# Kernel optimization log

Hardware: AMD Instinct MI355X
Metric: run time of the kernel (lower is better)

Reference implementation:

```python
import jax, jax.numpy as jnp
import numpy as np

NUM_HEADS = 16


def setup_inputs() -> dict:
    key = jax.random.key(0)
    k1, _ = jax.random.split(key)
    B, T, C = 2, 2048, 1024
    x = jax.random.normal(k1, (B, T, C), dtype=jnp.float32)
    r_sigma = jnp.array([0.01], dtype=jnp.float32)  # learned scalar, init 0.01
    return {"x": x, "r_sigma": r_sigma}


def reference(x, r_sigma):
    B, T, C = x.shape
    H = NUM_HEADS
    hd = C // H
    xh = x.reshape(B, T, H, hd)                      # (B,T,H,hd)
    # expand_dims(x,2) - expand_dims(x,3): pairwise diff across the HEAD axis
    diff = xh[:, :, None, :, :] - xh[:, :, :, None, :]   # (B,T,H,H,hd)
    # Dist**2 == sum of squared diffs (avoid sqrt-then-square; same math)
    dist_sq = jnp.sum(diff * diff, axis=-1)          # (B,T,H,H)
    Kmat = jnp.exp(-dist_sq * r_sigma[0])            # Gaussian kernel
    # y = x + K @ x  (contract over second head axis)
    y = xh + jnp.einsum('bthg,btgd->bthd', Kmat, xh)
    return y.reshape(B, T, C)
```

## Files before the change

### kernel.cpp

```cpp
#include <hip/hip_runtime.h>


#define NH 16
#define HD 64
#define CC 1024

__global__ __launch_bounds__(256) void K_attention_MH_kernel(
    const float* __restrict__ x,
    const float* __restrict__ r_sigma,
    float* __restrict__ y) {
  __shared__ float xs[HD * 17];
  __shared__ float Ks[NH * NH];

  const int tok = blockIdx.x;
  const int tid = threadIdx.x;
  const float* xp = x + (size_t)tok * CC;
  float* yp = y + (size_t)tok * CC;
  const float sigma = r_sigma[0];

  const float4 v = reinterpret_cast<const float4*>(xp)[tid];
  const int base = tid * 4;
  const int h = base >> 6;
  const int d0 = base & 63;
  xs[(d0 + 0) * 17 + h] = v.x;
  xs[(d0 + 1) * 17 + h] = v.y;
  xs[(d0 + 2) * 17 + h] = v.z;
  xs[(d0 + 3) * 17 + h] = v.w;
  __syncthreads();

  {
    const int hh = tid >> 4;
    const int gg = tid & 15;
    float acc = 0.0f;
#pragma unroll
    for (int d = 0; d < HD; ++d) {
      const float a = xs[d * 17 + hh];
      const float b = xs[d * 17 + gg];
      const float diff = a - b;
      acc = fmaf(diff, diff, acc);
    }
    Ks[hh * 16 + gg] = __expf(-acc * sigma);
  }
  __syncthreads();

  float s0 = 0.0f, s1 = 0.0f, s2 = 0.0f, s3 = 0.0f;
#pragma unroll
  for (int g = 0; g < NH; ++g) {
    const float k = Ks[h * 16 + g];
    s0 = fmaf(k, xs[(d0 + 0) * 17 + g], s0);
    s1 = fmaf(k, xs[(d0 + 1) * 17 + g], s1);
    s2 = fmaf(k, xs[(d0 + 2) * 17 + g], s2);
    s3 = fmaf(k, xs[(d0 + 3) * 17 + g], s3);
  }
  float4 o;
  o.x = v.x + s0;
  o.y = v.y + s1;
  o.z = v.z + s2;
  o.w = v.w + s3;
  reinterpret_cast<float4*>(yp)[tid] = o;
}

extern "C" void kernel_launch(void* const* d_in, const int* in_sizes, int n_in,
                              void* d_out, int out_size, void* d_ws, size_t ws_size,
                              hipStream_t stream) {
  const float* x = (const float*)d_in[0];
  const float* r_sigma = (const float*)d_in[1];
  float* out = (float*)d_out;
  const int ntok = in_sizes[0] / CC;
  K_attention_MH_kernel<<<ntok, 256, 0, stream>>>(x, r_sigma, out);
}
```

Baseline: 81.99 us.

## Compute per-token Gram and K@x with fp16 MFMA, one wave per token

Each wavefront now handles a single token, so block-wide __syncthreads become wave barriers. The pairwise squared distances are computed as |a|^2+|b|^2-2ab from a 16x16 Gram matrix produced by an fp16 MFMA. The K@x product also runs on MFMA in fp16. This moves the scalar FMA loops onto matrix units and cuts synchronisation cost, but casting to fp16 and the Gram expansion lose precision, and the output stores are no longer float4-vectorised.

```diff
diff --git a/kernel.cpp b/kernel.cpp
--- a/kernel.cpp
+++ b/kernel.cpp
@@ -4,60 +4,92 @@
 #define NH 16
 #define HD 64
 #define CC 1024
+#define LDSROW 68
+
+typedef float  f32x4 __attribute__((ext_vector_type(4)));
+typedef _Float16 f16x4 __attribute__((ext_vector_type(4)));
+typedef _Float16 f16x8 __attribute__((ext_vector_type(8)));
 
 __global__ __launch_bounds__(256) void K_attention_MH_kernel(
     const float* __restrict__ x,
     const float* __restrict__ r_sigma,
-    float* __restrict__ y) {
-  __shared__ float xs[HD * 17];
-  __shared__ float Ks[NH * NH];
+    float* __restrict__ y,
+    int ntok) {
+  __shared__ __align__(16) float xs[4][NH * LDSROW];
+  __shared__ __align__(16) float diag[4][NH];
 
-  const int tok = blockIdx.x;
-  const int tid = threadIdx.x;
+  const int wid  = threadIdx.x >> 6;
+  const int lane = threadIdx.x & 63;
+  const int tok  = blockIdx.x * 4 + wid;
+  if (tok >= ntok) return;
+
   const float* xp = x + (size_t)tok * CC;
-  float* yp = y + (size_t)tok * CC;
+  float*       yp = y + (size_t)tok * CC;
+  float* xw = xs[wid];
+  float* dw = diag[wid];
   const float sigma = r_sigma[0];
 
-  const float4 v = reinterpret_cast<const float4*>(xp)[tid];
-  const int base = tid * 4;
-  const int h = base >> 6;
-  const int d0 = base & 63;
-  xs[(d0 + 0) * 17 + h] = v.x;
-  xs[(d0 + 1) * 17 + h] = v.y;
-  xs[(d0 + 2) * 17 + h] = v.z;
-  xs[(d0 + 3) * 17 + h] = v.w;
-  __syncthreads();
+  const int q   = lane >> 4;
+  const int col = lane & 15;
 
-  {
-    const int hh = tid >> 4;
-    const int gg = tid & 15;
-    float acc = 0.0f;
 #pragma unroll
-    for (int d = 0; d < HD; ++d) {
-      const float a = xs[d * 17 + hh];
-      const float b = xs[d * 17 + gg];
-      const float diff = a - b;
-      acc = fmaf(diff, diff, acc);
+  for (int i = 0; i < 4; ++i) {
+    const float4 v = reinterpret_cast<const float4*>(xp)[lane + 64 * i];
+    const int p = (lane + 64 * i) * 4;
+    const int h = p >> 6, d = p & 63;
+    *reinterpret_cast<float4*>(&xw[h * LDSROW + d]) = v;
+  }
+  __builtin_amdgcn_wave_barrier();
+
+  f32x4 g = {0.f, 0.f, 0.f, 0.f};
+#pragma unroll
+  for (int kc = 0; kc < 2; ++kc) {
+    const float4 a0 = *reinterpret_cast<const float4*>(&xw[col * LDSROW + 8 * q + 32 * kc]);
+    const float4 a1 = *reinterpret_cast<const float4*>(&xw[col * LDSROW + 8 * q + 32 * kc + 4]);
+    f16x8 af;
+    af[0] = (_Float16)a0.x; af[1] = (_Float16)a0.y;
+    af[2] = (_Float16)a0.z; af[3] = (_Float16)a0.w;
+    af[4] = (_Float16)a1.x; af[5] = (_Float16)a1.y;
+    af[6] = (_Float16)a1.z; af[7] = (_Float16)a1.w;
+    g = __builtin_amdgcn_mfma_f32_16x16x32_f16(af, af, g, 0, 0, 0);
+  }
+
+  if ((col >> 2) == q) {
+    const int rsel = col & 3;
+    const float dv = (rsel == 0) ? g[0] : (rsel == 1) ? g[1] : (rsel == 2) ? g[2] : g[3];
+    dw[col] = dv;
+  }
+  __builtin_amdgcn_wave_barrier();
+  const float dgc = dw[col];
+  const f32x4 dh  = *reinterpret_cast<const f32x4*>(&dw[4 * q]);
+
+  f16x4 ka;
+  f32x4 kv;
+#pragma unroll
+  for (int r = 0; r < 4; ++r) {
+    const float d2 = dh[r] + dgc - 2.0f * g[r];
+    const float kvr = __expf(-sigma * d2);
+    kv[r] = kvr;
+    ka[r] = (_Float16)kvr;
+  }
+  (void)kv;
+
+#pragma unroll
+  for (int c = 0; c < 4; ++c) {
+    float xb[4];
+    f16x4 bfr;
+#pragma unroll
+    for (int j = 0; j < 4; ++j) {
+      xb[j]  = xw[(4 * q + j) * LDSROW + 16 * c + col];
+      bfr[j] = (_Float16)xb[j];
     }
-    Ks[hh * 16 + gg] = __expf(-acc * sigma);
+    f32x4 acc = {0.f, 0.f, 0.f, 0.f};
+    acc = __builtin_amdgcn_mfma_f32_16x16x16f16(ka, bfr, acc, 0, 0, 0);
+#pragma unroll
+    for (int r = 0; r < 4; ++r) {
+      yp[(4 * q + r) * HD + 16 * c + col] = xb[r] + acc[r];
+    }
   }
-  __syncthreads();
-
-  float s0 = 0.0f, s1 = 0.0f, s2 = 0.0f, s3 = 0.0f;
-#pragma unroll
-  for (int g = 0; g < NH; ++g) {
-    const float k = Ks[h * 16 + g];
-    s0 = fmaf(k, xs[(d0 + 0) * 17 + g], s0);
-    s1 = fmaf(k, xs[(d0 + 1) * 17 + g], s1);
-    s2 = fmaf(k, xs[(d0 + 2) * 17 + g], s2);
-    s3 = fmaf(k, xs[(d0 + 3) * 17 + g], s3);
-  }
-  float4 o;
-  o.x = v.x + s0;
-  o.y = v.y + s1;
-  o.z = v.z + s2;
-  o.w = v.w + s3;
-  reinterpret_cast<float4*>(yp)[tid] = o;
 }
 
 extern "C" void kernel_launch(void* const* d_in, const int* in_sizes, int n_in,
@@ -67,5 +99,6 @@
   const float* r_sigma = (const float*)d_in[1];
   float* out = (float*)d_out;
   const int ntok = in_sizes[0] / CC;
-  K_attention_MH_kernel<<<ntok, 256, 0, stream>>>(x, r_sigma, out);
+  const int blocks = (ntok + 3) / 4;
+  K_attention_MH_kernel<<<blocks, 256, 0, stream>>>(x, r_sigma, out, ntok);
 }
```

Result: faster. 69.37 us (-15.4%).
